# Performance work log

Measured on AMD Instinct MI355X. Metric: run time of the kernel, lower is better.

Reference implementation:

```python
import jax, jax.numpy as jnp
import numpy as np

T, H, I = 8192, 4096, 11008  # tokens, hidden, intermediate (LLaMA-7B)


def setup_inputs() -> dict:
    key = jax.random.key(0)
    ks = jax.random.split(key, 8)
    # int8-valued tensors stored as int32 (spec dtype enum lacks int8)
    hidden_states = jax.random.randint(ks[0], (T, H), -128, 128, dtype=jnp.int32)
    gate_w = jax.random.randint(ks[1], (I, H), -128, 128, dtype=jnp.int32)
    up_w = jax.random.randint(ks[2], (I, H), -128, 128, dtype=jnp.int32)
    down_w = jax.random.randint(ks[3], (H, I), -128, 128, dtype=jnp.int32)
    # per-tensor dequant scales (alpha = input_scale * weight_scale); small so
    # the SwiGLU product lands roughly in int8 range before requantization
    gate_a = jnp.float32(0.004)
    up_a = jnp.float32(0.004)
    down_a = jnp.float32(0.004)
    gate_b = jax.random.normal(ks[4], (I,), dtype=jnp.float32)
    up_b = jax.random.normal(ks[5], (I,), dtype=jnp.float32)
    down_b = jax.random.normal(ks[6], (H,), dtype=jnp.float32)
    return dict(hidden_states=hidden_states, gate_w=gate_w, gate_a=gate_a,
                gate_b=gate_b, up_w=up_w, up_a=up_a, up_b=up_b,
                down_w=down_w, down_a=down_a, down_b=down_b)


def _w8a8_linear(x_i8, w_i8, alpha, bias):
    # scale alpha and fp32 bias (W8A8BFP32OFP32Linear semantics).
    acc = jnp.matmul(x_i8.astype(jnp.int8), w_i8.astype(jnp.int8).T,
                     preferred_element_type=jnp.int32)
    return acc.astype(jnp.float32) * alpha + bias


def reference(hidden_states, gate_w, gate_a, gate_b, up_w, up_a, up_b,
              down_w, down_a, down_b):
    x1 = jax.nn.silu(_w8a8_linear(hidden_states, gate_w, gate_a, gate_b))  # [T,I]
    x2 = _w8a8_linear(hidden_states, up_w, up_a, up_b)                     # [T,I]
    x = x1 * x2
    # requantize: round, clamp to int8 range
    q = jnp.clip(jnp.round(x), -128.0, 127.0).astype(jnp.int32)
    return _w8a8_linear(q, down_w, down_a, down_b)                          # [T,H]
```

## Files before the change

kernel.cpp:

```cpp
#include <hip/hip_runtime.h>
#include <math.h>

#define T_DIM 8192
#define H_DIM 4096
#define I_DIM 11008

typedef int v4i  __attribute__((ext_vector_type(4)));
typedef int v16i __attribute__((ext_vector_type(16)));

#define MFMA8 __builtin_amdgcn_mfma_i32_32x32x32_i8

#define AS1(p) ((const __attribute__((address_space(1))) void*)(p))
#define AS3(p) ((__attribute__((address_space(3))) void*)(p))

#define WAITV(N) do { asm volatile("s_waitcnt vmcnt(" #N ")" ::: "memory"); \
                      __builtin_amdgcn_sched_barrier(0); } while (0)
#define BAR() __builtin_amdgcn_s_barrier()
#define LGKM(N) do { asm volatile("s_waitcnt lgkmcnt(" #N ")" ::: "memory"); \
                     __builtin_amdgcn_sched_barrier(0); } while (0)

__device__ __forceinline__ v4i DSR(const char* p) {
  v4i r;
  unsigned a = (unsigned)(size_t)(const __attribute__((address_space(3))) char*)p;
  asm volatile("ds_read_b128 %0, %1" : "=v"(r) : "v"(a));
  return r;
}

#define STG(ldst, gsrc) \
  __builtin_amdgcn_global_load_lds(AS1(gsrc), AS3(ldst), 16, 0, 0)

__global__ void pack_shuf(const int* __restrict__ src, char* __restrict__ dst,
                          int nk32, long nchunk) {
  long c = (long)blockIdx.x * blockDim.x + threadIdx.x;
  long stride = (long)gridDim.x * blockDim.x;
  for (; c < nchunk; c += stride) {
    int lane = (int)(c & 63);
    long rk = c >> 6;
    long r32 = rk / nk32;
    int k32 = (int)(rk - r32 * nk32);
    const int4* s = (const int4*)(src + (r32 * 32 + (lane & 31)) * (long)(nk32 * 32)
                                      + (long)k32 * 32 + ((lane >> 5) << 4));
    int4 a = s[0], b = s[1], cc = s[2], d = s[3];
    int w0 = (a.x & 255) | ((a.y & 255) << 8) | ((a.z & 255) << 16) | (a.w << 24);
    int w1 = (b.x & 255) | ((b.y & 255) << 8) | ((b.z & 255) << 16) | (b.w << 24);
    int w2 = (cc.x & 255) | ((cc.y & 255) << 8) | ((cc.z & 255) << 16) | (cc.w << 24);
    int w3 = (d.x & 255) | ((d.y & 255) << 8) | ((d.z & 255) << 16) | (d.w << 24);
    ((int4*)dst)[c] = make_int4(w0, w1, w2, w3);
  }
}

__global__ __launch_bounds__(512, 2) void gemm_gateup(
    const char* __restrict__ A, const char* __restrict__ Bg, const char* __restrict__ Bu,
    const float* __restrict__ ga_p, const float* __restrict__ gb,
    const float* __restrict__ ua_p, const float* __restrict__ ub,
    char* __restrict__ Q)
{
  __shared__ char lds[3][32768];
  const int tid = threadIdx.x;
  const int l = tid & 63;
  const int w = tid >> 6;
  const int wm = w >> 2, wn = w & 3;
  const int li32 = l & 31, kg2 = l >> 5;

  const int q8 = 2752 / 8;
  int bid = blockIdx.x;
  int wgid = (bid & 7) * q8 + (bid >> 3);
  int st = wgid >> 3, r = wgid & 7;
  int sm = st / 43, sn = st - sm * 43;
  const int m0 = (sm * 4 + (r & 3)) * 256;
  const int n0 = (sn * 2 + (r >> 2)) * 128;

  const int NK = H_DIM / 32;
  const int NT = H_DIM / 64;

  v16i accg[4], accu[4];
#pragma unroll
  for (int i = 0; i < 4; ++i)
#pragma unroll
    for (int j = 0; j < 16; ++j) { accg[i][j] = 0; accu[i][j] = 0; }

  const int lo = l * 16;
  const char* pA0 = A  + ((size_t)((m0 >> 5) + w) * NK + 0) * 1024 + lo;
  const char* pA1 = A  + ((size_t)((m0 >> 5) + w) * NK + 1) * 1024 + lo;
  const char* pG  = Bg + ((size_t)((n0 >> 5) + (w >> 1)) * NK + (w & 1)) * 1024 + lo;
  const char* pU  = Bu + ((size_t)((n0 >> 5) + (w >> 1)) * NK + (w & 1)) * 1024 + lo;
  const int dA0 = w * 2048 + lo;
  const int dA1 = dA0 + 1024;
  const int dG  = 16384 + w * 1024 + lo;
  const int dU  = dG + 8192;

#define STAGE_GU(SB, tt)                                                  \
  do {                                                                    \
    size_t so = (size_t)(tt) * 2048;                                      \
    STG((SB) + dA0, pA0 + so);                                            \
    STG((SB) + dA1, pA1 + so);                                            \
    STG((SB) + dG,  pG  + so);                                            \
    STG((SB) + dU,  pU  + so);                                            \
  } while (0)

  const int oA0 = (wm * 4 + 0) * 2048 + lo;
  const int oA1 = (wm * 4 + 1) * 2048 + lo;
  const int oA2 = (wm * 4 + 2) * 2048 + lo;
  const int oA3 = (wm * 4 + 3) * 2048 + lo;
  const int oG  = 16384 + wn * 2048 + lo;
  const int oU  = 24576 + wn * 2048 + lo;

  v4i E0, E1, E2, E3, Eg, Eu;
  v4i O0, O1, O2, O3, Og, Ou;

#define RD_GU(S, B, s)                                                    \
  do {                                                                    \
    S##0 = DSR((B) + oA0 + (s) * 1024);                                   \
    S##1 = DSR((B) + oA1 + (s) * 1024);                                   \
    S##2 = DSR((B) + oA2 + (s) * 1024);                                   \
    S##3 = DSR((B) + oA3 + (s) * 1024);                                   \
    S##g = DSR((B) + oG  + (s) * 1024);                                   \
    S##u = DSR((B) + oU  + (s) * 1024);                                   \
  } while (0)

#define MM_GU(S)                                                          \
  do {                                                                    \
    __builtin_amdgcn_s_setprio(1);                                        \
    accg[0] = MFMA8(S##0, S##g, accg[0], 0, 0, 0);                        \
    accu[0] = MFMA8(S##0, S##u, accu[0], 0, 0, 0);                        \
    accg[1] = MFMA8(S##1, S##g, accg[1], 0, 0, 0);                        \
    accu[1] = MFMA8(S##1, S##u, accu[1], 0, 0, 0);                        \
    accg[2] = MFMA8(S##2, S##g, accg[2], 0, 0, 0);                        \
    accu[2] = MFMA8(S##2, S##u, accu[2], 0, 0, 0);                        \
    accg[3] = MFMA8(S##3, S##g, accg[3], 0, 0, 0);                        \
    accu[3] = MFMA8(S##3, S##u, accu[3], 0, 0, 0);                        \
    __builtin_amdgcn_s_setprio(0);                                        \
  } while (0)

  char* b0 = lds[0];
  char* b1 = lds[1];
  char* b2 = lds[2];

  {
    STAGE_GU(b0, 0);
    STAGE_GU(b1, 1);
    WAITV(4);
    BAR();
    RD_GU(E, b0, 0);
  }

  for (int t = 0; t < NT; ++t) {
    const int tstage = (t + 2 < NT) ? (t + 2) : (NT - 1);
    RD_GU(O, b0, 1);
    STAGE_GU(b2, tstage);
    LGKM(6);
    MM_GU(E);
    WAITV(4);
    BAR();
    if (t + 1 < NT) {
      RD_GU(E, b1, 0);
      LGKM(6);
    } else {
      LGKM(0);
    }
    MM_GU(O);
    char* tmp = b0; b0 = b1; b1 = b2; b2 = tmp;
  }
  WAITV(0);
#undef RD_GU
#undef MM_GU
#undef STAGE_GU

  const float ga = *ga_p, ua = *ua_p;
  const int col = n0 + wn * 32 + li32;
  const float gbv = gb[col], ubv = ub[col];
  const int k32q = (n0 >> 5) + wn;
  const int lanehi = ((li32 >> 4) & 1) << 5;
  const int bytelo = li32 & 15;
  const int NKQ = I_DIM / 32;
#pragma unroll
  for (int mi = 0; mi < 4; ++mi) {
    const int r32q = (m0 >> 5) + wm * 4 + mi;
    char* qbase = Q + ((size_t)(r32q * NKQ + k32q) << 10);
#pragma unroll
    for (int rq = 0; rq < 4; ++rq) {
#pragma unroll
      for (int rr = 0; rr < 4; ++rr) {
        const int rg = rq * 4 + rr;
        const int rowin = kg2 * 4 + rq * 8 + rr;
        float g = (float)accg[mi][rg] * ga + gbv;
        float u = (float)accu[mi][rg] * ua + ubv;
        float x1 = g / (1.0f + expf(-g));
        float x = rintf(x1 * u);
        x = fminf(fmaxf(x, -128.0f), 127.0f);
        qbase[((rowin | lanehi) << 4) + bytelo] = (char)(int)x;
      }
    }
  }
}

__global__ __launch_bounds__(512, 2) void gemm_down(
    const char* __restrict__ Qm, const char* __restrict__ Bd,
    const float* __restrict__ da_p, const float* __restrict__ db,
    float* __restrict__ out)
{
  __shared__ char lds[3][32768];
  const int tid = threadIdx.x;
  const int l = tid & 63;
  const int w = tid >> 6;
  const int wm = w >> 2, wn = w & 3;
  const int li32 = l & 31, kg2 = l >> 5;

  const int q8 = 512 / 8;
  int bid = blockIdx.x;
  int wgid = (bid & 7) * q8 + (bid >> 3);
  int st = wgid >> 3, r = wgid & 7;
  int sm = st >> 3, sn = st & 7;
  const int m0 = (sm * 4 + (r & 3)) * 256;
  const int n0 = (sn * 2 + (r >> 2)) * 256;

  const int NK = I_DIM / 32;
  const int NT = I_DIM / 64;

  v16i acc[4][2];
#pragma unroll
  for (int i = 0; i < 4; ++i)
#pragma unroll
    for (int n = 0; n < 2; ++n)
#pragma unroll
      for (int j = 0; j < 16; ++j) acc[i][n][j] = 0;

  const int lo = l * 16;
  const char* pA0 = Qm + ((size_t)((m0 >> 5) + w) * NK + 0) * 1024 + lo;
  const char* pA1 = Qm + ((size_t)((m0 >> 5) + w) * NK + 1) * 1024 + lo;
  const char* pB0 = Bd + ((size_t)((n0 >> 5) + w) * NK + 0) * 1024 + lo;
  const char* pB1 = Bd + ((size_t)((n0 >> 5) + w) * NK + 1) * 1024 + lo;
  const int dA0 = w * 2048 + lo;
  const int dA1 = dA0 + 1024;
  const int dB0 = 16384 + w * 2048 + lo;
  const int dB1 = dB0 + 1024;

#define STAGE_DN(SB, tt)                                                  \
  do {                                                                    \
    size_t so = (size_t)(tt) * 2048;                                      \
    STG((SB) + dA0, pA0 + so);                                            \
    STG((SB) + dA1, pA1 + so);                                            \
    STG((SB) + dB0, pB0 + so);                                            \
    STG((SB) + dB1, pB1 + so);                                            \
  } while (0)

  const int oA0 = (wm * 4 + 0) * 2048 + lo;
  const int oA1 = (wm * 4 + 1) * 2048 + lo;
  const int oA2 = (wm * 4 + 2) * 2048 + lo;
  const int oA3 = (wm * 4 + 3) * 2048 + lo;
  const int oB0 = 16384 + (wn * 2 + 0) * 2048 + lo;
  const int oB1 = 16384 + (wn * 2 + 1) * 2048 + lo;

  v4i E0, E1, E2, E3, Eb0, Eb1;
  v4i O0, O1, O2, O3, Ob0, Ob1;

#define RD_DN(S, B, s)                                                    \
  do {                                                                    \
    S##0 = DSR((B) + oA0 + (s) * 1024);                                   \
    S##1 = DSR((B) + oA1 + (s) * 1024);                                   \
    S##2 = DSR((B) + oA2 + (s) * 1024);                                   \
    S##3 = DSR((B) + oA3 + (s) * 1024);                                   \
    S##b0 = DSR((B) + oB0 + (s) * 1024);                                  \
    S##b1 = DSR((B) + oB1 + (s) * 1024);                                  \
  } while (0)

#define MM_DN(S)                                                          \
  do {                                                                    \
    __builtin_amdgcn_s_setprio(1);                                        \
    acc[0][0] = MFMA8(S##0, S##b0, acc[0][0], 0, 0, 0);                   \
    acc[0][1] = MFMA8(S##0, S##b1, acc[0][1], 0, 0, 0);                   \
    acc[1][0] = MFMA8(S##1, S##b0, acc[1][0], 0, 0, 0);                   \
    acc[1][1] = MFMA8(S##1, S##b1, acc[1][1], 0, 0, 0);                   \
    acc[2][0] = MFMA8(S##2, S##b0, acc[2][0], 0, 0, 0);                   \
    acc[2][1] = MFMA8(S##2, S##b1, acc[2][1], 0, 0, 0);                   \
    acc[3][0] = MFMA8(S##3, S##b0, acc[3][0], 0, 0, 0);                   \
    acc[3][1] = MFMA8(S##3, S##b1, acc[3][1], 0, 0, 0);                   \
    __builtin_amdgcn_s_setprio(0);                                        \
  } while (0)

  char* b0 = lds[0];
  char* b1 = lds[1];
  char* b2 = lds[2];

  {
    STAGE_DN(b0, 0);
    STAGE_DN(b1, 1);
    WAITV(4);
    BAR();
    RD_DN(E, b0, 0);
  }

  for (int t = 0; t < NT; ++t) {
    const int tstage = (t + 2 < NT) ? (t + 2) : (NT - 1);
    RD_DN(O, b0, 1);
    STAGE_DN(b2, tstage);
    LGKM(6);
    MM_DN(E);

    WAITV(4);
    BAR();
    if (t + 1 < NT) {
      RD_DN(E, b1, 0);
      LGKM(6);
    } else {
      LGKM(0);
    }
    MM_DN(O);

    char* tmp = b0; b0 = b1; b1 = b2; b2 = tmp;
  }
  WAITV(0);
#undef RD_DN
#undef MM_DN
#undef STAGE_DN

  const float da = *da_p;
#pragma unroll
  for (int ni = 0; ni < 2; ++ni) {
    const int col = n0 + wn * 64 + ni * 32 + li32;
    const float dbv = db[col];
#pragma unroll
    for (int mi = 0; mi < 4; ++mi) {
      const int rowb = m0 + wm * 128 + mi * 32 + kg2 * 4;
#pragma unroll
      for (int rq = 0; rq < 4; ++rq) {
#pragma unroll
        for (int rr = 0; rr < 4; ++rr)
          out[(size_t)(rowb + rq * 8 + rr) * H_DIM + col] =
              (float)acc[mi][ni][rq * 4 + rr] * da + dbv;
      }
    }
  }
}

extern "C" void kernel_launch(void* const* d_in, const int* in_sizes, int n_in,
                              void* d_out, int out_size, void* d_ws, size_t ws_size,
                              hipStream_t stream) {
  const int*   hs = (const int*)d_in[0];
  const int*   gw = (const int*)d_in[1];
  const float* ga = (const float*)d_in[2];
  const float* gb = (const float*)d_in[3];
  const int*   uw = (const int*)d_in[4];
  const float* ua = (const float*)d_in[5];
  const float* ub = (const float*)d_in[6];
  const int*   dw = (const int*)d_in[7];
  const float* da = (const float*)d_in[8];
  const float* db = (const float*)d_in[9];

  char* ws   = (char*)d_ws;
  char* hidS = ws;
  char* gS   = hidS + (size_t)T_DIM * H_DIM;
  char* uS   = gS   + (size_t)I_DIM * H_DIM;
  char* dS   = uS   + (size_t)I_DIM * H_DIM;
  char* qS   = dS   + (size_t)H_DIM * I_DIM;

  pack_shuf<<<2048, 256, 0, stream>>>(hs, hidS, H_DIM / 32, (long)T_DIM * H_DIM / 16);
  pack_shuf<<<2048, 256, 0, stream>>>(gw, gS,   H_DIM / 32, (long)I_DIM * H_DIM / 16);
  pack_shuf<<<2048, 256, 0, stream>>>(uw, uS,   H_DIM / 32, (long)I_DIM * H_DIM / 16);
  pack_shuf<<<2048, 256, 0, stream>>>(dw, dS,   I_DIM / 32, (long)H_DIM * I_DIM / 16);

  gemm_gateup<<<2752, 512, 0, stream>>>(hidS, gS, uS, ga, gb, ua, ub, qS);
  gemm_down<<<512, 512, 0, stream>>>(qS, dS, da, db, (float*)d_out);
}
```

Baseline: 1.089 ms.

## Load GEMM B fragments directly into registers, stage only A through LDS

```diff
diff --git a/kernel.cpp b/kernel.cpp
--- a/kernel.cpp
+++ b/kernel.cpp
@@ -18,12 +18,19 @@
 #define BAR() __builtin_amdgcn_s_barrier()
 #define LGKM(N) do { asm volatile("s_waitcnt lgkmcnt(" #N ")" ::: "memory"); \
                      __builtin_amdgcn_sched_barrier(0); } while (0)
+#define SCHEDB() __builtin_amdgcn_sched_barrier(0)
 
 __device__ __forceinline__ v4i DSR(const char* p) {
   v4i r;
   unsigned a = (unsigned)(size_t)(const __attribute__((address_space(3))) char*)p;
   asm volatile("ds_read_b128 %0, %1" : "=v"(r) : "v"(a));
   return r;
+}
+
+__device__ __forceinline__ const char* rflp(const void* p) {
+  unsigned lo = __builtin_amdgcn_readfirstlane((unsigned)(unsigned long long)p);
+  unsigned hi = __builtin_amdgcn_readfirstlane((unsigned)((unsigned long long)p >> 32));
+  return (const char*)(((unsigned long long)hi << 32) | lo);
 }
 
 #define STG(ldst, gsrc) \
@@ -55,7 +62,7 @@
     const float* __restrict__ ua_p, const float* __restrict__ ub,
     char* __restrict__ Q)
 {
-  __shared__ char lds[3][32768];
+  __shared__ char lds[3][16384];
   const int tid = threadIdx.x;
   const int l = tid & 63;
   const int w = tid >> 6;
@@ -80,55 +87,55 @@
     for (int j = 0; j < 16; ++j) { accg[i][j] = 0; accu[i][j] = 0; }
 
   const int lo = l * 16;
-  const char* pA0 = A  + ((size_t)((m0 >> 5) + w) * NK + 0) * 1024 + lo;
-  const char* pA1 = A  + ((size_t)((m0 >> 5) + w) * NK + 1) * 1024 + lo;
-  const char* pG  = Bg + ((size_t)((n0 >> 5) + (w >> 1)) * NK + (w & 1)) * 1024 + lo;
-  const char* pU  = Bu + ((size_t)((n0 >> 5) + (w >> 1)) * NK + (w & 1)) * 1024 + lo;
+  const char* pA0 = A + ((size_t)((m0 >> 5) + w) * NK) * 1024 + lo;
   const int dA0 = w * 2048 + lo;
   const int dA1 = dA0 + 1024;
-  const int dG  = 16384 + w * 1024 + lo;
-  const int dU  = dG + 8192;
-
-#define STAGE_GU(SB, tt)                                                  \
+
+#define STAGE_A(SB, tt)                                                   \
   do {                                                                    \
     size_t so = (size_t)(tt) * 2048;                                      \
     STG((SB) + dA0, pA0 + so);                                            \
-    STG((SB) + dA1, pA1 + so);                                            \
-    STG((SB) + dG,  pG  + so);                                            \
-    STG((SB) + dU,  pU  + so);                                            \
+    STG((SB) + dA1, pA0 + so + 1024);                                     \
+  } while (0)
+
+  const char* bG = rflp(Bg + ((size_t)((n0 >> 5) + wn) * NK) * 1024);
+  const char* bU = rflp(Bu + ((size_t)((n0 >> 5) + wn) * NK) * 1024);
+
+#define LDB_GU(G0, U0, G1, U1, tt)                                        \
+  do {                                                                    \
+    size_t ko = (size_t)(tt) * 2048 + lo;                                 \
+    G0 = *(const v4i*)(bG + ko);        U0 = *(const v4i*)(bU + ko);      \
+    G1 = *(const v4i*)(bG + ko + 1024); U1 = *(const v4i*)(bU + ko + 1024);\
+    SCHEDB();                                                             \
   } while (0)
 
   const int oA0 = (wm * 4 + 0) * 2048 + lo;
   const int oA1 = (wm * 4 + 1) * 2048 + lo;
   const int oA2 = (wm * 4 + 2) * 2048 + lo;
   const int oA3 = (wm * 4 + 3) * 2048 + lo;
-  const int oG  = 16384 + wn * 2048 + lo;
-  const int oU  = 24576 + wn * 2048 + lo;
-
-  v4i E0, E1, E2, E3, Eg, Eu;
-  v4i O0, O1, O2, O3, Og, Ou;
-
-#define RD_GU(S, B, s)                                                    \
+
+  v4i E0, E1, E2, E3;
+  v4i O0, O1, O2, O3;
+
+#define RD_A(S, B, s)                                                     \
   do {                                                                    \
     S##0 = DSR((B) + oA0 + (s) * 1024);                                   \
     S##1 = DSR((B) + oA1 + (s) * 1024);                                   \
     S##2 = DSR((B) + oA2 + (s) * 1024);                                   \
     S##3 = DSR((B) + oA3 + (s) * 1024);                                   \
-    S##g = DSR((B) + oG  + (s) * 1024);                                   \
-    S##u = DSR((B) + oU  + (s) * 1024);                                   \
-  } while (0)
-
-#define MM_GU(S)                                                          \
+  } while (0)
+
+#define MM_GU(S, Gf, Uf)                                                  \
   do {                                                                    \
     __builtin_amdgcn_s_setprio(1);                                        \
-    accg[0] = MFMA8(S##0, S##g, accg[0], 0, 0, 0);                        \
-    accu[0] = MFMA8(S##0, S##u, accu[0], 0, 0, 0);                        \
-    accg[1] = MFMA8(S##1, S##g, accg[1], 0, 0, 0);                        \
-    accu[1] = MFMA8(S##1, S##u, accu[1], 0, 0, 0);                        \
-    accg[2] = MFMA8(S##2, S##g, accg[2], 0, 0, 0);                        \
-    accu[2] = MFMA8(S##2, S##u, accu[2], 0, 0, 0);                        \
-    accg[3] = MFMA8(S##3, S##g, accg[3], 0, 0, 0);                        \
-    accu[3] = MFMA8(S##3, S##u, accu[3], 0, 0, 0);                        \
+    accg[0] = MFMA8(S##0, Gf, accg[0], 0, 0, 0);                          \
+    accu[0] = MFMA8(S##0, Uf, accu[0], 0, 0, 0);                          \
+    accg[1] = MFMA8(S##1, Gf, accg[1], 0, 0, 0);                          \
+    accu[1] = MFMA8(S##1, Uf, accu[1], 0, 0, 0);                          \
+    accg[2] = MFMA8(S##2, Gf, accg[2], 0, 0, 0);                          \
+    accu[2] = MFMA8(S##2, Uf, accu[2], 0, 0, 0);                          \
+    accg[3] = MFMA8(S##3, Gf, accg[3], 0, 0, 0);                          \
+    accu[3] = MFMA8(S##3, Uf, accu[3], 0, 0, 0);                          \
     __builtin_amdgcn_s_setprio(0);                                        \
   } while (0)
 
@@ -136,35 +143,45 @@
   char* b1 = lds[1];
   char* b2 = lds[2];
 
+  v4i GA0, UA0, GA1, UA1;
+  v4i GB0, UB0, GB1, UB1;
+
   {
-    STAGE_GU(b0, 0);
-    STAGE_GU(b1, 1);
-    WAITV(4);
+    STAGE_A(b0, 0);
+    STAGE_A(b1, 1);
+    LDB_GU(GA0, UA0, GA1, UA1, 0);
+    LDB_GU(GB0, UB0, GB1, UB1, 1);
+    WAITV(0);
     BAR();
-    RD_GU(E, b0, 0);
-  }
-
-  for (int t = 0; t < NT; ++t) {
-    const int tstage = (t + 2 < NT) ? (t + 2) : (NT - 1);
-    RD_GU(O, b0, 1);
-    STAGE_GU(b2, tstage);
-    LGKM(6);
-    MM_GU(E);
-    WAITV(4);
-    BAR();
-    if (t + 1 < NT) {
-      RD_GU(E, b1, 0);
-      LGKM(6);
-    } else {
-      LGKM(0);
-    }
-    MM_GU(O);
-    char* tmp = b0; b0 = b1; b1 = b2; b2 = tmp;
+    RD_A(E, b0, 0);
+  }
+
+#define BODY_GU(t, G0, U0, G1, U1)                                        \
+  do {                                                                    \
+    const int ts = ((t) + 2 < NT) ? ((t) + 2) : (NT - 1);                 \
+    RD_A(O, b0, 1);                                                       \
+    STAGE_A(b2, ts);                                                      \
+    LGKM(4);                                                              \
+    MM_GU(E, G0, U0);                                                     \
+    WAITV(2);                                                             \
+    BAR();                                                                \
+    RD_A(E, b1, 0);                                                       \
+    LGKM(4);                                                              \
+    MM_GU(O, G1, U1);                                                     \
+    LDB_GU(G0, U0, G1, U1, ts);                                           \
+    char* tmp_ = b0; b0 = b1; b1 = b2; b2 = tmp_;                         \
+  } while (0)
+
+  for (int tt = 0; tt < NT; tt += 2) {
+    BODY_GU(tt,     GA0, UA0, GA1, UA1);
+    BODY_GU(tt + 1, GB0, UB0, GB1, UB1);
   }
   WAITV(0);
-#undef RD_GU
+#undef BODY_GU
+#undef RD_A
 #undef MM_GU
-#undef STAGE_GU
+#undef STAGE_A
+#undef LDB_GU
 
   const float ga = *ga_p, ua = *ua_p;
   const int col = n0 + wn * 32 + li32;
@@ -199,7 +216,7 @@
     const float* __restrict__ da_p, const float* __restrict__ db,
     float* __restrict__ out)
 {
-  __shared__ char lds[3][32768];
+  __shared__ char lds[3][16384];
   const int tid = threadIdx.x;
   const int l = tid & 63;
   const int w = tid >> 6;
@@ -226,55 +243,55 @@
       for (int j = 0; j < 16; ++j) acc[i][n][j] = 0;
 
   const int lo = l * 16;
-  const char* pA0 = Qm + ((size_t)((m0 >> 5) + w) * NK + 0) * 1024 + lo;
-  const char* pA1 = Qm + ((size_t)((m0 >> 5) + w) * NK + 1) * 1024 + lo;
-  const char* pB0 = Bd + ((size_t)((n0 >> 5) + w) * NK + 0) * 1024 + lo;
-  const char* pB1 = Bd + ((size_t)((n0 >> 5) + w) * NK + 1) * 1024 + lo;
+  const char* pA0 = Qm + ((size_t)((m0 >> 5) + w) * NK) * 1024 + lo;
   const int dA0 = w * 2048 + lo;
   const int dA1 = dA0 + 1024;
-  const int dB0 = 16384 + w * 2048 + lo;
-  const int dB1 = dB0 + 1024;
-
-#define STAGE_DN(SB, tt)                                                  \
+
+#define STAGE_A(SB, tt)                                                   \
   do {                                                                    \
     size_t so = (size_t)(tt) * 2048;                                      \
     STG((SB) + dA0, pA0 + so);                                            \
-    STG((SB) + dA1, pA1 + so);                                            \
-    STG((SB) + dB0, pB0 + so);                                            \
-    STG((SB) + dB1, pB1 + so);                                            \
+    STG((SB) + dA1, pA0 + so + 1024);                                     \
+  } while (0)
+
+  const char* bB0 = rflp(Bd + ((size_t)((n0 >> 5) + wn * 2 + 0) * NK) * 1024);
+  const char* bB1 = rflp(Bd + ((size_t)((n0 >> 5) + wn * 2 + 1) * NK) * 1024);
+
+#define LDB_DN(X0, Y0, X1, Y1, tt)                                        \
+  do {                                                                    \
+    size_t ko = (size_t)(tt) * 2048 + lo;                                 \
+    X0 = *(const v4i*)(bB0 + ko);        Y0 = *(const v4i*)(bB1 + ko);    \
+    X1 = *(const v4i*)(bB0 + ko + 1024); Y1 = *(const v4i*)(bB1 + ko + 1024);\
+    SCHEDB();                                                             \
   } while (0)
 
   const int oA0 = (wm * 4 + 0) * 2048 + lo;
   const int oA1 = (wm * 4 + 1) * 2048 + lo;
   const int oA2 = (wm * 4 + 2) * 2048 + lo;
   const int oA3 = (wm * 4 + 3) * 2048 + lo;
-  const int oB0 = 16384 + (wn * 2 + 0) * 2048 + lo;
-  const int oB1 = 16384 + (wn * 2 + 1) * 2048 + lo;
-
-  v4i E0, E1, E2, E3, Eb0, Eb1;
-  v4i O0, O1, O2, O3, Ob0, Ob1;
-
-#define RD_DN(S, B, s)                                                    \
+
+  v4i E0, E1, E2, E3;
+  v4i O0, O1, O2, O3;
+
+#define RD_A(S, B, s)                                                     \
   do {                                                                    \
     S##0 = DSR((B) + oA0 + (s) * 1024);                                   \
     S##1 = DSR((B) + oA1 + (s) * 1024);                                   \
     S##2 = DSR((B) + oA2 + (s) * 1024);                                   \
     S##3 = DSR((B) + oA3 + (s) * 1024);                                   \
-    S##b0 = DSR((B) + oB0 + (s) * 1024);                                  \
-    S##b1 = DSR((B) + oB1 + (s) * 1024);                                  \
-  } while (0)
-
-#define MM_DN(S)                                                          \
+  } while (0)
+
+#define MM_DN(S, Bx, By)                                                  \
   do {                                                                    \
     __builtin_amdgcn_s_setprio(1);                                        \
-    acc[0][0] = MFMA8(S##0, S##b0, acc[0][0], 0, 0, 0);                   \
-    acc[0][1] = MFMA8(S##0, S##b1, acc[0][1], 0, 0, 0);                   \
-    acc[1][0] = MFMA8(S##1, S##b0, acc[1][0], 0, 0, 0);                   \
-    acc[1][1] = MFMA8(S##1, S##b1, acc[1][1], 0, 0, 0);                   \
-    acc[2][0] = MFMA8(S##2, S##b0, acc[2][0], 0, 0, 0);                   \
-    acc[2][1] = MFMA8(S##2, S##b1, acc[2][1], 0, 0, 0);                   \
-    acc[3][0] = MFMA8(S##3, S##b0, acc[3][0], 0, 0, 0);                   \
-    acc[3][1] = MFMA8(S##3, S##b1, acc[3][1], 0, 0, 0);                   \
+    acc[0][0] = MFMA8(S##0, Bx, acc[0][0], 0, 0, 0);                      \
+    acc[0][1] = MFMA8(S##0, By, acc[0][1], 0, 0, 0);                      \
+    acc[1][0] = MFMA8(S##1, Bx, acc[1][0], 0, 0, 0);                      \
+    acc[1][1] = MFMA8(S##1, By, acc[1][1], 0, 0, 0);                      \
+    acc[2][0] = MFMA8(S##2, Bx, acc[2][0], 0, 0, 0);                      \
+    acc[2][1] = MFMA8(S##2, By, acc[2][1], 0, 0, 0);                      \
+    acc[3][0] = MFMA8(S##3, Bx, acc[3][0], 0, 0, 0);                      \
+    acc[3][1] = MFMA8(S##3, By, acc[3][1], 0, 0, 0);                      \
     __builtin_amdgcn_s_setprio(0);                                        \
   } while (0)
 
@@ -282,37 +299,45 @@
   char* b1 = lds[1];
   char* b2 = lds[2];
 
+  v4i XA0, YA0, XA1, YA1;
+  v4i XB0, YB0, XB1, YB1;
+
   {
-    STAGE_DN(b0, 0);
-    STAGE_DN(b1, 1);
-    WAITV(4);
+    STAGE_A(b0, 0);
+    STAGE_A(b1, 1);
+    LDB_DN(XA0, YA0, XA1, YA1, 0);
+    LDB_DN(XB0, YB0, XB1, YB1, 1);
+    WAITV(0);
     BAR();
-    RD_DN(E, b0, 0);
-  }
-
-  for (int t = 0; t < NT; ++t) {
-    const int tstage = (t + 2 < NT) ? (t + 2) : (NT - 1);
-    RD_DN(O, b0, 1);
-    STAGE_DN(b2, tstage);
-    LGKM(6);
-    MM_DN(E);
-
-    WAITV(4);
-    BAR();
-    if (t + 1 < NT) {
-      RD_DN(E, b1, 0);
-      LGKM(6);
-    } else {
-      LGKM(0);
-    }
-    MM_DN(O);
-
-    char* tmp = b0; b0 = b1; b1 = b2; b2 = tmp;
+    RD_A(E, b0, 0);
+  }
+
+#define BODY_DN(t, X0, Y0, X1, Y1)                                        \
+  do {                                                                    \
+    const int ts = ((t) + 2 < NT) ? ((t) + 2) : (NT - 1);                 \
+    RD_A(O, b0, 1);                                                       \
+    STAGE_A(b2, ts);                                                      \
+    LGKM(4);                                                              \
+    MM_DN(E, X0, Y0);                                                     \
+    WAITV(2);                                                             \
+    BAR();                                                                \
+    RD_A(E, b1, 0);                                                       \
+    LGKM(4);                                                              \
+    MM_DN(O, X1, Y1);                                                     \
+    LDB_DN(X0, Y0, X1, Y1, ts);                                           \
+    char* tmp_ = b0; b0 = b1; b1 = b2; b2 = tmp_;                         \
+  } while (0)
+
+  for (int tt = 0; tt < NT; tt += 2) {
+    BODY_DN(tt,     XA0, YA0, XA1, YA1);
+    BODY_DN(tt + 1, XB0, YB0, XB1, YB1);
   }
   WAITV(0);
-#undef RD_DN
+#undef BODY_DN
+#undef RD_A
 #undef MM_DN
-#undef STAGE_DN
+#undef STAGE_A
+#undef LDB_DN
 
   const float da = *da_p;
 #pragma unroll
```

Result: slower. 1.482 ms (+36.0%).

## Halve waves per block and double per-wave MFMA tile in both GEMMs

Applied to the files above, without the earlier changes.

```diff
diff --git a/kernel.cpp b/kernel.cpp
--- a/kernel.cpp
+++ b/kernel.cpp
@@ -49,7 +49,7 @@
   }
 }
 
-__global__ __launch_bounds__(512, 2) void gemm_gateup(
+__global__ __launch_bounds__(256, 1) void gemm_gateup(
     const char* __restrict__ A, const char* __restrict__ Bg, const char* __restrict__ Bu,
     const float* __restrict__ ga_p, const float* __restrict__ gb,
     const float* __restrict__ ua_p, const float* __restrict__ ub,
@@ -59,7 +59,7 @@
   const int tid = threadIdx.x;
   const int l = tid & 63;
   const int w = tid >> 6;
-  const int wm = w >> 2, wn = w & 3;
+  const int wm = w >> 1, wn = w & 1;
   const int li32 = l & 31, kg2 = l >> 5;
 
   const int q8 = 2752 / 8;
@@ -73,40 +73,47 @@
   const int NK = H_DIM / 32;
   const int NT = H_DIM / 64;
 
-  v16i accg[4], accu[4];
+  v16i accg[4][2], accu[4][2];
 #pragma unroll
   for (int i = 0; i < 4; ++i)
 #pragma unroll
-    for (int j = 0; j < 16; ++j) { accg[i][j] = 0; accu[i][j] = 0; }
+    for (int n = 0; n < 2; ++n)
+#pragma unroll
+      for (int j = 0; j < 16; ++j) { accg[i][n][j] = 0; accu[i][n][j] = 0; }
 
   const int lo = l * 16;
-  const char* pA0 = A  + ((size_t)((m0 >> 5) + w) * NK + 0) * 1024 + lo;
-  const char* pA1 = A  + ((size_t)((m0 >> 5) + w) * NK + 1) * 1024 + lo;
-  const char* pG  = Bg + ((size_t)((n0 >> 5) + (w >> 1)) * NK + (w & 1)) * 1024 + lo;
-  const char* pU  = Bu + ((size_t)((n0 >> 5) + (w >> 1)) * NK + (w & 1)) * 1024 + lo;
-  const int dA0 = w * 2048 + lo;
-  const int dA1 = dA0 + 1024;
-  const int dG  = 16384 + w * 1024 + lo;
-  const int dU  = dG + 8192;
+  const char* pA0 = A  + ((size_t)((m0 >> 5) + 2 * w)     * NK) * 1024 + lo;
+  const char* pA1 = A  + ((size_t)((m0 >> 5) + 2 * w + 1) * NK) * 1024 + lo;
+  const char* pG  = Bg + ((size_t)((n0 >> 5) + w) * NK) * 1024 + lo;
+  const char* pU  = Bu + ((size_t)((n0 >> 5) + w) * NK) * 1024 + lo;
+  const int dA = w * 4096 + lo;
+  const int dG = 16384 + w * 2048 + lo;
+  const int dU = 24576 + w * 2048 + lo;
 
 #define STAGE_GU(SB, tt)                                                  \
   do {                                                                    \
     size_t so = (size_t)(tt) * 2048;                                      \
-    STG((SB) + dA0, pA0 + so);                                            \
-    STG((SB) + dA1, pA1 + so);                                            \
-    STG((SB) + dG,  pG  + so);                                            \
-    STG((SB) + dU,  pU  + so);                                            \
+    STG((SB) + dA,        pA0 + so);                                      \
+    STG((SB) + dA + 1024, pA0 + so + 1024);                               \
+    STG((SB) + dA + 2048, pA1 + so);                                      \
+    STG((SB) + dA + 3072, pA1 + so + 1024);                               \
+    STG((SB) + dG,        pG + so);                                       \
+    STG((SB) + dG + 1024, pG + so + 1024);                                \
+    STG((SB) + dU,        pU + so);                                       \
+    STG((SB) + dU + 1024, pU + so + 1024);                                \
   } while (0)
 
   const int oA0 = (wm * 4 + 0) * 2048 + lo;
   const int oA1 = (wm * 4 + 1) * 2048 + lo;
   const int oA2 = (wm * 4 + 2) * 2048 + lo;
   const int oA3 = (wm * 4 + 3) * 2048 + lo;
-  const int oG  = 16384 + wn * 2048 + lo;
-  const int oU  = 24576 + wn * 2048 + lo;
-
-  v4i E0, E1, E2, E3, Eg, Eu;
-  v4i O0, O1, O2, O3, Og, Ou;
+  const int oG0 = 16384 + (wn * 2 + 0) * 2048 + lo;
+  const int oG1 = 16384 + (wn * 2 + 1) * 2048 + lo;
+  const int oU0 = 24576 + (wn * 2 + 0) * 2048 + lo;
+  const int oU1 = 24576 + (wn * 2 + 1) * 2048 + lo;
+
+  v4i E0, E1, E2, E3, Eg0, Eg1, Eu0, Eu1;
+  v4i O0, O1, O2, O3, Og0, Og1, Ou0, Ou1;
 
 #define RD_GU(S, B, s)                                                    \
   do {                                                                    \
@@ -114,21 +121,31 @@
     S##1 = DSR((B) + oA1 + (s) * 1024);                                   \
     S##2 = DSR((B) + oA2 + (s) * 1024);                                   \
     S##3 = DSR((B) + oA3 + (s) * 1024);                                   \
-    S##g = DSR((B) + oG  + (s) * 1024);                                   \
-    S##u = DSR((B) + oU  + (s) * 1024);                                   \
+    S##g0 = DSR((B) + oG0 + (s) * 1024);                                  \
+    S##g1 = DSR((B) + oG1 + (s) * 1024);                                  \
+    S##u0 = DSR((B) + oU0 + (s) * 1024);                                  \
+    S##u1 = DSR((B) + oU1 + (s) * 1024);                                  \
   } while (0)
 
 #define MM_GU(S)                                                          \
   do {                                                                    \
     __builtin_amdgcn_s_setprio(1);                                        \
-    accg[0] = MFMA8(S##0, S##g, accg[0], 0, 0, 0);                        \
-    accu[0] = MFMA8(S##0, S##u, accu[0], 0, 0, 0);                        \
-    accg[1] = MFMA8(S##1, S##g, accg[1], 0, 0, 0);                        \
-    accu[1] = MFMA8(S##1, S##u, accu[1], 0, 0, 0);                        \
-    accg[2] = MFMA8(S##2, S##g, accg[2], 0, 0, 0);                        \
-    accu[2] = MFMA8(S##2, S##u, accu[2], 0, 0, 0);                        \
-    accg[3] = MFMA8(S##3, S##g, accg[3], 0, 0, 0);                        \
-    accu[3] = MFMA8(S##3, S##u, accu[3], 0, 0, 0);                        \
+    accg[0][0] = MFMA8(S##0, S##g0, accg[0][0], 0, 0, 0);                 \
+    accg[0][1] = MFMA8(S##0, S##g1, accg[0][1], 0, 0, 0);                 \
+    accu[0][0] = MFMA8(S##0, S##u0, accu[0][0], 0, 0, 0);                 \
+    accu[0][1] = MFMA8(S##0, S##u1, accu[0][1], 0, 0, 0);                 \
+    accg[1][0] = MFMA8(S##1, S##g0, accg[1][0], 0, 0, 0);                 \
+    accg[1][1] = MFMA8(S##1, S##g1, accg[1][1], 0, 0, 0);                 \
+    accu[1][0] = MFMA8(S##1, S##u0, accu[1][0], 0, 0, 0);                 \
+    accu[1][1] = MFMA8(S##1, S##u1, accu[1][1], 0, 0, 0);                 \
+    accg[2][0] = MFMA8(S##2, S##g0, accg[2][0], 0, 0, 0);                 \
+    accg[2][1] = MFMA8(S##2, S##g1, accg[2][1], 0, 0, 0);                 \
+    accu[2][0] = MFMA8(S##2, S##u0, accu[2][0], 0, 0, 0);                 \
+    accu[2][1] = MFMA8(S##2, S##u1, accu[2][1], 0, 0, 0);                 \
+    accg[3][0] = MFMA8(S##3, S##g0, accg[3][0], 0, 0, 0);                 \
+    accg[3][1] = MFMA8(S##3, S##g1, accg[3][1], 0, 0, 0);                 \
+    accu[3][0] = MFMA8(S##3, S##u0, accu[3][0], 0, 0, 0);                 \
+    accu[3][1] = MFMA8(S##3, S##u1, accu[3][1], 0, 0, 0);                 \
     __builtin_amdgcn_s_setprio(0);                                        \
   } while (0)
 
@@ -139,25 +156,21 @@
   {
     STAGE_GU(b0, 0);
     STAGE_GU(b1, 1);
-    WAITV(4);
+    WAITV(8);
     BAR();
     RD_GU(E, b0, 0);
   }
 
   for (int t = 0; t < NT; ++t) {
-    const int tstage = (t + 2 < NT) ? (t + 2) : (NT - 1);
+    const int ts = (t + 2 < NT) ? (t + 2) : (NT - 1);
     RD_GU(O, b0, 1);
-    STAGE_GU(b2, tstage);
-    LGKM(6);
+    STAGE_GU(b2, ts);
+    LGKM(8);
     MM_GU(E);
-    WAITV(4);
+    WAITV(8);
+    LGKM(0);
     BAR();
-    if (t + 1 < NT) {
-      RD_GU(E, b1, 0);
-      LGKM(6);
-    } else {
-      LGKM(0);
-    }
+    RD_GU(E, b1, 0);
     MM_GU(O);
     char* tmp = b0; b0 = b1; b1 = b2; b2 = tmp;
   }
@@ -167,34 +180,37 @@
 #undef STAGE_GU
 
   const float ga = *ga_p, ua = *ua_p;
-  const int col = n0 + wn * 32 + li32;
-  const float gbv = gb[col], ubv = ub[col];
-  const int k32q = (n0 >> 5) + wn;
   const int lanehi = ((li32 >> 4) & 1) << 5;
   const int bytelo = li32 & 15;
   const int NKQ = I_DIM / 32;
 #pragma unroll
-  for (int mi = 0; mi < 4; ++mi) {
-    const int r32q = (m0 >> 5) + wm * 4 + mi;
-    char* qbase = Q + ((size_t)(r32q * NKQ + k32q) << 10);
-#pragma unroll
-    for (int rq = 0; rq < 4; ++rq) {
-#pragma unroll
-      for (int rr = 0; rr < 4; ++rr) {
-        const int rg = rq * 4 + rr;
-        const int rowin = kg2 * 4 + rq * 8 + rr;
-        float g = (float)accg[mi][rg] * ga + gbv;
-        float u = (float)accu[mi][rg] * ua + ubv;
-        float x1 = g / (1.0f + expf(-g));
-        float x = rintf(x1 * u);
-        x = fminf(fmaxf(x, -128.0f), 127.0f);
-        qbase[((rowin | lanehi) << 4) + bytelo] = (char)(int)x;
+  for (int ni = 0; ni < 2; ++ni) {
+    const int col = n0 + wn * 64 + ni * 32 + li32;
+    const float gbv = gb[col], ubv = ub[col];
+    const int k32q = (n0 >> 5) + wn * 2 + ni;
+#pragma unroll
+    for (int mi = 0; mi < 4; ++mi) {
+      const int r32q = (m0 >> 5) + wm * 4 + mi;
+      char* qbase = Q + ((size_t)(r32q * NKQ + k32q) << 10);
+#pragma unroll
+      for (int rq = 0; rq < 4; ++rq) {
+#pragma unroll
+        for (int rr = 0; rr < 4; ++rr) {
+          const int rg = rq * 4 + rr;
+          const int rowin = kg2 * 4 + rq * 8 + rr;
+          float g = (float)accg[mi][ni][rg] * ga + gbv;
+          float u = (float)accu[mi][ni][rg] * ua + ubv;
+          float x1 = g / (1.0f + expf(-g));
+          float x = rintf(x1 * u);
+          x = fminf(fmaxf(x, -128.0f), 127.0f);
+          qbase[((rowin | lanehi) << 4) + bytelo] = (char)(int)x;
+        }
       }
     }
   }
 }
 
-__global__ __launch_bounds__(512, 2) void gemm_down(
+__global__ __launch_bounds__(256, 1) void gemm_down(
     const char* __restrict__ Qm, const char* __restrict__ Bd,
     const float* __restrict__ da_p, const float* __restrict__ db,
     float* __restrict__ out)
@@ -203,7 +219,7 @@
   const int tid = threadIdx.x;
   const int l = tid & 63;
   const int w = tid >> 6;
-  const int wm = w >> 2, wn = w & 3;
+  const int wm = w >> 1, wn = w & 1;
   const int li32 = l & 31, kg2 = l >> 5;
 
   const int q8 = 512 / 8;
@@ -217,42 +233,46 @@
   const int NK = I_DIM / 32;
   const int NT = I_DIM / 64;
 
-  v16i acc[4][2];
+  v16i acc[4][4];
 #pragma unroll
   for (int i = 0; i < 4; ++i)
 #pragma unroll
-    for (int n = 0; n < 2; ++n)
+    for (int n = 0; n < 4; ++n)
 #pragma unroll
       for (int j = 0; j < 16; ++j) acc[i][n][j] = 0;
 
   const int lo = l * 16;
-  const char* pA0 = Qm + ((size_t)((m0 >> 5) + w) * NK + 0) * 1024 + lo;
-  const char* pA1 = Qm + ((size_t)((m0 >> 5) + w) * NK + 1) * 1024 + lo;
-  const char* pB0 = Bd + ((size_t)((n0 >> 5) + w) * NK + 0) * 1024 + lo;
-  const char* pB1 = Bd + ((size_t)((n0 >> 5) + w) * NK + 1) * 1024 + lo;
-  const int dA0 = w * 2048 + lo;
-  const int dA1 = dA0 + 1024;
-  const int dB0 = 16384 + w * 2048 + lo;
-  const int dB1 = dB0 + 1024;
+  const char* pA0 = Qm + ((size_t)((m0 >> 5) + 2 * w)     * NK) * 1024 + lo;
+  const char* pA1 = Qm + ((size_t)((m0 >> 5) + 2 * w + 1) * NK) * 1024 + lo;
+  const char* pB0 = Bd + ((size_t)((n0 >> 5) + 2 * w)     * NK) * 1024 + lo;
+  const char* pB1 = Bd + ((size_t)((n0 >> 5) + 2 * w + 1) * NK) * 1024 + lo;
+  const int dA = w * 4096 + lo;
+  const int dB = 16384 + w * 4096 + lo;
 
 #define STAGE_DN(SB, tt)                                                  \
   do {                                                                    \
     size_t so = (size_t)(tt) * 2048;                                      \
-    STG((SB) + dA0, pA0 + so);                                            \
-    STG((SB) + dA1, pA1 + so);                                            \
-    STG((SB) + dB0, pB0 + so);                                            \
-    STG((SB) + dB1, pB1 + so);                                            \
+    STG((SB) + dA,        pA0 + so);                                      \
+    STG((SB) + dA + 1024, pA0 + so + 1024);                               \
+    STG((SB) + dA + 2048, pA1 + so);                                      \
+    STG((SB) + dA + 3072, pA1 + so + 1024);                               \
+    STG((SB) + dB,        pB0 + so);                                      \
+    STG((SB) + dB + 1024, pB0 + so + 1024);                               \
+    STG((SB) + dB + 2048, pB1 + so);                                      \
+    STG((SB) + dB + 3072, pB1 + so + 1024);                               \
   } while (0)
 
   const int oA0 = (wm * 4 + 0) * 2048 + lo;
   const int oA1 = (wm * 4 + 1) * 2048 + lo;
   const int oA2 = (wm * 4 + 2) * 2048 + lo;
   const int oA3 = (wm * 4 + 3) * 2048 + lo;
-  const int oB0 = 16384 + (wn * 2 + 0) * 2048 + lo;
-  const int oB1 = 16384 + (wn * 2 + 1) * 2048 + lo;
-
-  v4i E0, E1, E2, E3, Eb0, Eb1;
-  v4i O0, O1, O2, O3, Ob0, Ob1;
+  const int oB0 = 16384 + (wn * 4 + 0) * 2048 + lo;
+  const int oB1 = 16384 + (wn * 4 + 1) * 2048 + lo;
+  const int oB2 = 16384 + (wn * 4 + 2) * 2048 + lo;
+  const int oB3 = 16384 + (wn * 4 + 3) * 2048 + lo;
+
+  v4i E0, E1, E2, E3, Eb0, Eb1, Eb2, Eb3;
+  v4i O0, O1, O2, O3, Ob0, Ob1, Ob2, Ob3;
 
 #define RD_DN(S, B, s)                                                    \
   do {                                                                    \
@@ -262,6 +282,8 @@
     S##3 = DSR((B) + oA3 + (s) * 1024);                                   \
     S##b0 = DSR((B) + oB0 + (s) * 1024);                                  \
     S##b1 = DSR((B) + oB1 + (s) * 1024);                                  \
+    S##b2 = DSR((B) + oB2 + (s) * 1024);                                  \
+    S##b3 = DSR((B) + oB3 + (s) * 1024);                                  \
   } while (0)
 
 #define MM_DN(S)                                                          \
@@ -269,12 +291,20 @@
     __builtin_amdgcn_s_setprio(1);                                        \
     acc[0][0] = MFMA8(S##0, S##b0, acc[0][0], 0, 0, 0);                   \
     acc[0][1] = MFMA8(S##0, S##b1, acc[0][1], 0, 0, 0);                   \
+    acc[0][2] = MFMA8(S##0, S##b2, acc[0][2], 0, 0, 0);                   \
+    acc[0][3] = MFMA8(S##0, S##b3, acc[0][3], 0, 0, 0);                   \
     acc[1][0] = MFMA8(S##1, S##b0, acc[1][0], 0, 0, 0);                   \
     acc[1][1] = MFMA8(S##1, S##b1, acc[1][1], 0, 0, 0);                   \
+    acc[1][2] = MFMA8(S##1, S##b2, acc[1][2], 0, 0, 0);                   \
+    acc[1][3] = MFMA8(S##1, S##b3, acc[1][3], 0, 0, 0);                   \
     acc[2][0] = MFMA8(S##2, S##b0, acc[2][0], 0, 0, 0);                   \
     acc[2][1] = MFMA8(S##2, S##b1, acc[2][1], 0, 0, 0);                   \
+    acc[2][2] = MFMA8(S##2, S##b2, acc[2][2], 0, 0, 0);                   \
+    acc[2][3] = MFMA8(S##2, S##b3, acc[2][3], 0, 0, 0);                   \
     acc[3][0] = MFMA8(S##3, S##b0, acc[3][0], 0, 0, 0);                   \
     acc[3][1] = MFMA8(S##3, S##b1, acc[3][1], 0, 0, 0);                   \
+    acc[3][2] = MFMA8(S##3, S##b2, acc[3][2], 0, 0, 0);                   \
+    acc[3][3] = MFMA8(S##3, S##b3, acc[3][3], 0, 0, 0);                   \
     __builtin_amdgcn_s_setprio(0);                                        \
   } while (0)
 
@@ -285,28 +315,23 @@
   {
     STAGE_DN(b0, 0);
     STAGE_DN(b1, 1);
-    WAITV(4);
+    WAITV(8);
     BAR();
     RD_DN(E, b0, 0);
   }
 
   for (int t = 0; t < NT; ++t) {
-    const int tstage = (t + 2 < NT) ? (t + 2) : (NT - 1);
+    const int ts = (t + 2 < NT) ? (t + 2) : (NT - 1);
     RD_DN(O, b0, 1);
-    STAGE_DN(b2, tstage);
-    LGKM(6);
+    STAGE_DN(b2, ts);
+    LGKM(8);
     MM_DN(E);
 
-    WAITV(4);
+    WAITV(8);
+    LGKM(0);
     BAR();
-    if (t + 1 < NT) {
-      RD_DN(E, b1, 0);
-      LGKM(6);
-    } else {
-      LGKM(0);
-    }
+    RD_DN(E, b1, 0);
     MM_DN(O);
-
     char* tmp = b0; b0 = b1; b1 = b2; b2 = tmp;
   }
   WAITV(0);
@@ -316,8 +341,8 @@
 
   const float da = *da_p;
 #pragma unroll
-  for (int ni = 0; ni < 2; ++ni) {
-    const int col = n0 + wn * 64 + ni * 32 + li32;
+  for (int ni = 0; ni < 4; ++ni) {
+    const int col = n0 + wn * 128 + ni * 32 + li32;
     const float dbv = db[col];
 #pragma unroll
     for (int mi = 0; mi < 4; ++mi) {
@@ -359,6 +384,6 @@
   pack_shuf<<<2048, 256, 0, stream>>>(uw, uS,   H_DIM / 32, (long)I_DIM * H_DIM / 16);
   pack_shuf<<<2048, 256, 0, stream>>>(dw, dS,   I_DIM / 32, (long)H_DIM * I_DIM / 16);
 
-  gemm_gateup<<<2752, 512, 0, stream>>>(hidS, gS, uS, ga, gb, ua, ub, qS);
-  gemm_down<<<512, 512, 0, stream>>>(qS, dS, da, db, (float*)d_out);
-}
+  gemm_gateup<<<2752, 256, 0, stream>>>(hidS, gS, uS, ga, gb, ua, ub, qS);
+  gemm_down<<<512, 256, 0, stream>>>(qS, dS, da, db, (float*)d_out);
+}
```

Measured after the change: 2.042 ms. 87.4% more time.

## Stagger K sub-step order across waves and simplify LDS read pipeline

Applied to the files above, without the earlier changes.

```diff
diff --git a/kernel.cpp b/kernel.cpp
--- a/kernel.cpp
+++ b/kernel.cpp
@@ -13,11 +13,10 @@
 #define AS1(p) ((const __attribute__((address_space(1))) void*)(p))
 #define AS3(p) ((__attribute__((address_space(3))) void*)(p))
 
-#define WAITV(N) do { asm volatile("s_waitcnt vmcnt(" #N ")" ::: "memory"); \
-                      __builtin_amdgcn_sched_barrier(0); } while (0)
+#define WAITV(N) asm volatile("s_waitcnt vmcnt(" #N ")" ::: "memory")
 #define BAR() __builtin_amdgcn_s_barrier()
-#define LGKM(N) do { asm volatile("s_waitcnt lgkmcnt(" #N ")" ::: "memory"); \
-                     __builtin_amdgcn_sched_barrier(0); } while (0)
+#define LGKM0 do { asm volatile("s_waitcnt lgkmcnt(0)" ::: "memory"); \
+                   __builtin_amdgcn_sched_barrier(0); } while (0)
 
 __device__ __forceinline__ v4i DSR(const char* p) {
   v4i r;
@@ -98,25 +97,24 @@
     STG((SB) + dU,  pU  + so);                                            \
   } while (0)
 
-  const int oA0 = (wm * 4 + 0) * 2048 + lo;
-  const int oA1 = (wm * 4 + 1) * 2048 + lo;
-  const int oA2 = (wm * 4 + 2) * 2048 + lo;
-  const int oA3 = (wm * 4 + 3) * 2048 + lo;
-  const int oG  = 16384 + wn * 2048 + lo;
-  const int oU  = 24576 + wn * 2048 + lo;
+  const int sF = (w < 4) ? 0 : 1;
+  const int sS = 1 - sF;
+
+  const int fA0 = (wm * 4 + 0) * 2048 + lo + sF * 1024;
+  const int fA1 = (wm * 4 + 1) * 2048 + lo + sF * 1024;
+  const int fA2 = (wm * 4 + 2) * 2048 + lo + sF * 1024;
+  const int fA3 = (wm * 4 + 3) * 2048 + lo + sF * 1024;
+  const int fG  = 16384 + wn * 2048 + lo + sF * 1024;
+  const int fU  = 24576 + wn * 2048 + lo + sF * 1024;
+  const int gA0 = (wm * 4 + 0) * 2048 + lo + sS * 1024;
+  const int gA1 = (wm * 4 + 1) * 2048 + lo + sS * 1024;
+  const int gA2 = (wm * 4 + 2) * 2048 + lo + sS * 1024;
+  const int gA3 = (wm * 4 + 3) * 2048 + lo + sS * 1024;
+  const int gG  = 16384 + wn * 2048 + lo + sS * 1024;
+  const int gU  = 24576 + wn * 2048 + lo + sS * 1024;
 
   v4i E0, E1, E2, E3, Eg, Eu;
   v4i O0, O1, O2, O3, Og, Ou;
-
-#define RD_GU(S, B, s)                                                    \
-  do {                                                                    \
-    S##0 = DSR((B) + oA0 + (s) * 1024);                                   \
-    S##1 = DSR((B) + oA1 + (s) * 1024);                                   \
-    S##2 = DSR((B) + oA2 + (s) * 1024);                                   \
-    S##3 = DSR((B) + oA3 + (s) * 1024);                                   \
-    S##g = DSR((B) + oG  + (s) * 1024);                                   \
-    S##u = DSR((B) + oU  + (s) * 1024);                                   \
-  } while (0)
 
 #define MM_GU(S)                                                          \
   do {                                                                    \
@@ -141,28 +139,26 @@
     STAGE_GU(b1, 1);
     WAITV(4);
     BAR();
-    RD_GU(E, b0, 0);
   }
 
   for (int t = 0; t < NT; ++t) {
-    const int tstage = (t + 2 < NT) ? (t + 2) : (NT - 1);
-    RD_GU(O, b0, 1);
-    STAGE_GU(b2, tstage);
-    LGKM(6);
+    const int ts = (t + 2 < NT) ? (t + 2) : (NT - 1);
+    E0 = DSR(b0 + fA0); E1 = DSR(b0 + fA1);
+    E2 = DSR(b0 + fA2); E3 = DSR(b0 + fA3);
+    Eg = DSR(b0 + fG);  Eu = DSR(b0 + fU);
+    STAGE_GU(b2, ts);
+    LGKM0;
     MM_GU(E);
+    O0 = DSR(b0 + gA0); O1 = DSR(b0 + gA1);
+    O2 = DSR(b0 + gA2); O3 = DSR(b0 + gA3);
+    Og = DSR(b0 + gG);  Ou = DSR(b0 + gU);
+    LGKM0;
+    MM_GU(O);
     WAITV(4);
     BAR();
-    if (t + 1 < NT) {
-      RD_GU(E, b1, 0);
-      LGKM(6);
-    } else {
-      LGKM(0);
-    }
-    MM_GU(O);
     char* tmp = b0; b0 = b1; b1 = b2; b2 = tmp;
   }
   WAITV(0);
-#undef RD_GU
 #undef MM_GU
 #undef STAGE_GU
 
@@ -244,25 +240,24 @@
     STG((SB) + dB1, pB1 + so);                                            \
   } while (0)
 
-  const int oA0 = (wm * 4 + 0) * 2048 + lo;
-  const int oA1 = (wm * 4 + 1) * 2048 + lo;
-  const int oA2 = (wm * 4 + 2) * 2048 + lo;
-  const int oA3 = (wm * 4 + 3) * 2048 + lo;
-  const int oB0 = 16384 + (wn * 2 + 0) * 2048 + lo;
-  const int oB1 = 16384 + (wn * 2 + 1) * 2048 + lo;
+  const int sF = (w < 4) ? 0 : 1;
+  const int sS = 1 - sF;
+
+  const int fA0 = (wm * 4 + 0) * 2048 + lo + sF * 1024;
+  const int fA1 = (wm * 4 + 1) * 2048 + lo + sF * 1024;
+  const int fA2 = (wm * 4 + 2) * 2048 + lo + sF * 1024;
+  const int fA3 = (wm * 4 + 3) * 2048 + lo + sF * 1024;
+  const int fB0 = 16384 + (wn * 2 + 0) * 2048 + lo + sF * 1024;
+  const int fB1 = 16384 + (wn * 2 + 1) * 2048 + lo + sF * 1024;
+  const int gA0 = (wm * 4 + 0) * 2048 + lo + sS * 1024;
+  const int gA1 = (wm * 4 + 1) * 2048 + lo + sS * 1024;
+  const int gA2 = (wm * 4 + 2) * 2048 + lo + sS * 1024;
+  const int gA3 = (wm * 4 + 3) * 2048 + lo + sS * 1024;
+  const int gB0 = 16384 + (wn * 2 + 0) * 2048 + lo + sS * 1024;
+  const int gB1 = 16384 + (wn * 2 + 1) * 2048 + lo + sS * 1024;
 
   v4i E0, E1, E2, E3, Eb0, Eb1;
   v4i O0, O1, O2, O3, Ob0, Ob1;
-
-#define RD_DN(S, B, s)                                                    \
-  do {                                                                    \
-    S##0 = DSR((B) + oA0 + (s) * 1024);                                   \
-    S##1 = DSR((B) + oA1 + (s) * 1024);                                   \
-    S##2 = DSR((B) + oA2 + (s) * 1024);                                   \
-    S##3 = DSR((B) + oA3 + (s) * 1024);                                   \
-    S##b0 = DSR((B) + oB0 + (s) * 1024);                                  \
-    S##b1 = DSR((B) + oB1 + (s) * 1024);                                  \
-  } while (0)
 
 #define MM_DN(S)                                                          \
   do {                                                                    \
@@ -287,30 +282,28 @@
     STAGE_DN(b1, 1);
     WAITV(4);
     BAR();
-    RD_DN(E, b0, 0);
   }
 
   for (int t = 0; t < NT; ++t) {
-    const int tstage = (t + 2 < NT) ? (t + 2) : (NT - 1);
-    RD_DN(O, b0, 1);
-    STAGE_DN(b2, tstage);
-    LGKM(6);
+    const int ts = (t + 2 < NT) ? (t + 2) : (NT - 1);
+    E0 = DSR(b0 + fA0);  E1 = DSR(b0 + fA1);
+    E2 = DSR(b0 + fA2);  E3 = DSR(b0 + fA3);
+    Eb0 = DSR(b0 + fB0); Eb1 = DSR(b0 + fB1);
+    STAGE_DN(b2, ts);
+    LGKM0;
     MM_DN(E);
+
+    O0 = DSR(b0 + gA0);  O1 = DSR(b0 + gA1);
+    O2 = DSR(b0 + gA2);  O3 = DSR(b0 + gA3);
+    Ob0 = DSR(b0 + gB0); Ob1 = DSR(b0 + gB1);
+    LGKM0;
+    MM_DN(O);
 
     WAITV(4);
     BAR();
-    if (t + 1 < NT) {
-      RD_DN(E, b1, 0);
-      LGKM(6);
-    } else {
-      LGKM(0);
-    }
-    MM_DN(O);
-
     char* tmp = b0; b0 = b1; b1 = b2; b2 = tmp;
   }
   WAITV(0);
-#undef RD_DN
 #undef MM_DN
 #undef STAGE_DN
 
```

New measurement: 1.178 ms. 8.2% more time.
